# Optimization experiments

Measured on AMD Instinct MI355X. Metric: run time of the kernel, lower is better.

Reference implementation:

```python
import jax, jax.numpy as jnp
import numpy as np

K = 8  # kernel_size
COUT = 512


def setup_inputs() -> dict:
    key = jax.random.key(0)
    k1, k2, k3 = jax.random.split(key, 3)
    B, CIN, L = 8, 512, 2048
    x = jax.random.normal(k1, (B, CIN, L), dtype=jnp.float32)
    # nn.Linear(CIN, COUT*K) weight, scaled like kaiming-uniform-ish init
    W = jax.random.normal(k2, (COUT * K, CIN), dtype=jnp.float32) * (1.0 / np.sqrt(CIN))
    b = jax.random.normal(k3, (COUT,), dtype=jnp.float32)
    return {"x": x, "W": W, "b": b}


def reference(x, W, b):
    # x: (B, Cin, L); W: (Cout*K, Cin) with row layout j = k*Cout + co; b: (Cout,)
    B, Cin, L = x.shape
    # pointwise linear expand: (B, Cout*K, L)
    z = jnp.einsum('bcl,oc->bol', x, W)
    z = z.reshape(B, K, COUT, L)  # k-major channel layout
    # causal overlap-add fold: y[b,co,t] = sum_k z[b,k,co,t-k]
    y = z[:, 0]
    for k in range(1, K):  # small fixed kernel-size loop
        y = y.at[:, :, k:].add(z[:, k, :, : L - k])
    return y + b[None, :, None]
```

## Files before the change

### kernel.cpp

```cpp
#include <hip/hip_runtime.h>
#include <hip/hip_bf16.h>
#include <cstdint>
#include <cstddef>

#define CIN   512
#define COUT  512
#define LLEN  2048
#define BATCH 8
#define KTAP  8
#define LPAD  (LLEN + 8)

typedef __bf16 bf16x8_t __attribute__((ext_vector_type(8)));
typedef float  f32x4_t  __attribute__((ext_vector_type(4)));
typedef unsigned short u16x8_t __attribute__((ext_vector_type(8)));

__device__ __forceinline__ unsigned short f2bf(float f) {
  __bf16 h = (__bf16)f;
  return __builtin_bit_cast(unsigned short, h);
}

__device__ __forceinline__ void gl2lds16(unsigned short* lds, const unsigned short* g) {
  __builtin_amdgcn_global_load_lds(
      (const __attribute__((address_space(1))) unsigned int*)g,
      (__attribute__((address_space(3))) unsigned int*)lds,
      16, 0, 0);
}


__global__ void convert_w_kernel(const float4* __restrict__ W, u16x8_t* __restrict__ Wb) {
  int idx = blockIdx.x * 256 + threadIdx.x;
  float4 a = W[idx * 2], b = W[idx * 2 + 1];
  u16x8_t o;
  o[0] = f2bf(a.x); o[1] = f2bf(a.y); o[2] = f2bf(a.z); o[3] = f2bf(a.w);
  o[4] = f2bf(b.x); o[5] = f2bf(b.y); o[6] = f2bf(b.z); o[7] = f2bf(b.w);
  Wb[idx] = o;
}

__global__ __launch_bounds__(256) void transpose_x_kernel(
    const float* __restrict__ x, unsigned short* __restrict__ xtp) {
  __shared__ float tile[64][65];
  const int t  = threadIdx.x;
  const int b  = blockIdx.z;
  const int c0 = blockIdx.y * 64;
  const int l0 = blockIdx.x * 64;

  if (blockIdx.x == 0 && t < 64) {
    unsigned short* hp = xtp + ((size_t)b * LPAD + (t >> 3)) * CIN + c0 + (t & 7) * 8;
    *(u16x8_t*)hp = (u16x8_t){0, 0, 0, 0, 0, 0, 0, 0};
  }

  {
    const int cr = t >> 2;
    const int lv = (t & 3) * 16;
    const float* src = x + ((size_t)b * CIN + c0 + cr) * LLEN + l0 + lv;
#pragma unroll
    for (int i = 0; i < 4; ++i) {
      float4 v = *(const float4*)(src + 4 * i);
      tile[cr][lv + 4 * i + 0] = v.x;
      tile[cr][lv + 4 * i + 1] = v.y;
      tile[cr][lv + 4 * i + 2] = v.z;
      tile[cr][lv + 4 * i + 3] = v.w;
    }
  }
  __syncthreads();

  {
    const int l    = t >> 2;
    const int cseg = (t & 3) * 16;
    unsigned short ov[16];
#pragma unroll
    for (int u = 0; u < 16; ++u) ov[u] = f2bf(tile[cseg + u][l]);
    unsigned short* dst = xtp + ((size_t)b * LPAD + 8 + l0 + l) * CIN + c0 + cseg;
    *(u16x8_t*)dst       = *(const u16x8_t*)&ov[0];
    *(u16x8_t*)(dst + 8) = *(const u16x8_t*)&ov[8];
  }
}


__global__ __launch_bounds__(256) void conv_gemm_kernel(
    const unsigned short* __restrict__ Wb,
    const unsigned short* __restrict__ xtp,
    const float* __restrict__ bias,
    float* __restrict__ y)
{
  __shared__ __align__(16) unsigned short As[128 * 64];
  __shared__ __align__(16) unsigned short Bs[136 * 64];

  const int t    = threadIdx.x;
  const int lane = t & 63;
  const int wid  = t >> 6;
  const int wm   = wid & 1, wn = wid >> 1;
  const int l0   = blockIdx.x * 128;
  const int o0   = blockIdx.y * 128;
  const int b    = blockIdx.z;

  const int quad = lane >> 4;
  const int lrow = lane & 15;

  f32x4_t acc[4][4];
#pragma unroll
  for (int i = 0; i < 4; ++i)
#pragma unroll
    for (int j = 0; j < 4; ++j)
      acc[i][j] = (f32x4_t){0.f, 0.f, 0.f, 0.f};

  const int srow    = t >> 3;
  const int schunk  = (t & 7) ^ (srow & 7);
  const int lds_off = t * 8;

  const unsigned short* xb = xtp + (size_t)b * LPAD * CIN;

#pragma unroll 1
  for (int ct = 0; ct < 8; ++ct) {
    const int c0 = ct * 64;
    {
      const unsigned short* src = xb + (size_t)(l0 + srow) * CIN + c0 + schunk * 8;
#pragma unroll
      for (int rd = 0; rd < 4; ++rd)
        gl2lds16(Bs + lds_off + rd * 2048, src + (size_t)rd * 32 * CIN);
      if (t < 64) {
        const int r2 = 128 + (t >> 3);
        const int ch2 = (t & 7) ^ (r2 & 7);
        gl2lds16(Bs + 128 * 64 + t * 8,
                 xb + (size_t)(l0 + r2) * CIN + c0 + ch2 * 8);
      }
    }
#pragma unroll
    for (int k = 0; k < 8; ++k) {
      const unsigned short* asrc =
          Wb + (size_t)(k * COUT + o0 + srow) * CIN + c0 + schunk * 8;
#pragma unroll
      for (int rd = 0; rd < 4; ++rd)
        gl2lds16(As + lds_off + rd * 2048, asrc + (size_t)rd * 32 * CIN);
      __syncthreads();

#pragma unroll
      for (int h = 0; h < 2; ++h) {
        bf16x8_t af[4], bfr[4];
#pragma unroll
        for (int i = 0; i < 4; ++i) {
          int row  = wm * 64 + i * 16 + lrow;
          int slot = (h * 4 + quad) ^ (row & 7);
          af[i] = *(const bf16x8_t*)(As + row * 64 + slot * 8);
        }
#pragma unroll
        for (int j = 0; j < 4; ++j) {
          int row  = (8 - k) + wn * 64 + j * 16 + lrow;
          int slot = (h * 4 + quad) ^ (row & 7);
          bfr[j] = *(const bf16x8_t*)(Bs + row * 64 + slot * 8);
        }
#pragma unroll
        for (int i = 0; i < 4; ++i)
#pragma unroll
          for (int j = 0; j < 4; ++j)
            acc[i][j] = __builtin_amdgcn_mfma_f32_16x16x32_bf16(af[i], bfr[j], acc[i][j], 0, 0, 0);
      }
      __syncthreads();
    }
  }

#pragma unroll
  for (int i = 0; i < 4; ++i) {
    const int o_base = o0 + wm * 64 + i * 16 + quad * 4;
    const float4 bv = *(const float4*)(bias + o_base);
    const float bvr[4] = {bv.x, bv.y, bv.z, bv.w};
#pragma unroll
    for (int j = 0; j < 4; ++j) {
      const int l = l0 + wn * 64 + j * 16 + lrow;
#pragma unroll
      for (int r = 0; r < 4; ++r) {
        y[((size_t)b * COUT + o_base + r) * LLEN + l] = acc[i][j][r] + bvr[r];
      }
    }
  }
}


extern "C" void kernel_launch(void* const* d_in, const int* in_sizes, int n_in,
                              void* d_out, int out_size, void* d_ws, size_t ws_size,
                              hipStream_t stream) {
  const float* x    = (const float*)d_in[0];
  const float* W    = (const float*)d_in[1];
  const float* bias = (const float*)d_in[2];
  float* y          = (float*)d_out;

  unsigned short* xtp = (unsigned short*)d_ws;
  unsigned short* Wb  = (unsigned short*)((char*)d_ws +
                        (size_t)BATCH * LPAD * CIN * sizeof(unsigned short));

  convert_w_kernel<<<(KTAP * COUT * CIN / 8) / 256, 256, 0, stream>>>(
      (const float4*)W, (u16x8_t*)Wb);
  transpose_x_kernel<<<dim3(LLEN / 64, CIN / 64, BATCH), 256, 0, stream>>>(x, xtp);
  conv_gemm_kernel<<<dim3(LLEN / 128, COUT / 128, BATCH), 256, 0, stream>>>(
      Wb, xtp, bias, y);
}
```

Baseline: 150.0 us.

## Load weight fragments directly to registers with prefetch and merge prepass kernels

The GEMM kernel stops staging the weight tile through LDS. Each wave now loads its own A fragments from global memory straight into registers, one k-step ahead (double-buffered registers), which removes the per-tap LDS writes and two barriers per tap. The weight conversion and x transpose kernels are merged into one launch to save launch overhead. The cost is higher register pressure and uncoalesced 16-byte global reads of W that rely on L2/cache hits, with each wave reloading weights that the other wn wave also loads.

New measurement: 211.5 us. 1.41x slower.

```diff
diff --git a/kernel.cpp b/kernel.cpp
--- a/kernel.cpp
+++ b/kernel.cpp
@@ -26,25 +26,28 @@
       16, 0, 0);
 }
 
-
-__global__ void convert_w_kernel(const float4* __restrict__ W, u16x8_t* __restrict__ Wb) {
-  int idx = blockIdx.x * 256 + threadIdx.x;
-  float4 a = W[idx * 2], b = W[idx * 2 + 1];
-  u16x8_t o;
-  o[0] = f2bf(a.x); o[1] = f2bf(a.y); o[2] = f2bf(a.z); o[3] = f2bf(a.w);
-  o[4] = f2bf(b.x); o[5] = f2bf(b.y); o[6] = f2bf(b.z); o[7] = f2bf(b.w);
-  Wb[idx] = o;
-}
-
-__global__ __launch_bounds__(256) void transpose_x_kernel(
-    const float* __restrict__ x, unsigned short* __restrict__ xtp) {
+__global__ __launch_bounds__(256) void prepass_kernel(
+    const float* __restrict__ x, unsigned short* __restrict__ xtp,
+    const float4* __restrict__ W, u16x8_t* __restrict__ Wb) {
+  const int bid = blockIdx.x;
+  const int t   = threadIdx.x;
+
+  if (bid >= 2048) {
+    int idx = (bid - 2048) * 256 + t;
+    float4 a = W[idx * 2], b = W[idx * 2 + 1];
+    u16x8_t o;
+    o[0] = f2bf(a.x); o[1] = f2bf(a.y); o[2] = f2bf(a.z); o[3] = f2bf(a.w);
+    o[4] = f2bf(b.x); o[5] = f2bf(b.y); o[6] = f2bf(b.z); o[7] = f2bf(b.w);
+    Wb[idx] = o;
+    return;
+  }
+
   __shared__ float tile[64][65];
-  const int t  = threadIdx.x;
-  const int b  = blockIdx.z;
-  const int c0 = blockIdx.y * 64;
-  const int l0 = blockIdx.x * 64;
-
-  if (blockIdx.x == 0 && t < 64) {
+  const int b  = bid >> 8;
+  const int c0 = ((bid >> 5) & 7) * 64;
+  const int l0 = (bid & 31) * 64;
+
+  if ((bid & 31) == 0 && t < 64) {
     unsigned short* hp = xtp + ((size_t)b * LPAD + (t >> 3)) * CIN + c0 + (t & 7) * 8;
     *(u16x8_t*)hp = (u16x8_t){0, 0, 0, 0, 0, 0, 0, 0};
   }
@@ -63,7 +66,6 @@
     }
   }
   __syncthreads();
-
   {
     const int l    = t >> 2;
     const int cseg = (t & 3) * 16;
@@ -83,7 +85,6 @@
     const float* __restrict__ bias,
     float* __restrict__ y)
 {
-  __shared__ __align__(16) unsigned short As[128 * 64];
   __shared__ __align__(16) unsigned short Bs[136 * 64];
 
   const int t    = threadIdx.x;
@@ -110,39 +111,49 @@
 
   const unsigned short* xb = xtp + (size_t)b * LPAD * CIN;
 
+  const unsigned short* aW =
+      Wb + ((size_t)o0 + wm * 64 + lrow) * CIN + quad * 8;
+
+  bf16x8_t afc[2][4], afn[2][4];
+#pragma unroll
+  for (int h = 0; h < 2; ++h)
+#pragma unroll
+    for (int i = 0; i < 4; ++i)
+      afc[h][i] = *(const bf16x8_t*)(aW + h * 32 + i * 16 * CIN);
+
 #pragma unroll 1
   for (int ct = 0; ct < 8; ++ct) {
     const int c0 = ct * 64;
+    if (ct) __syncthreads();
     {
       const unsigned short* src = xb + (size_t)(l0 + srow) * CIN + c0 + schunk * 8;
 #pragma unroll
       for (int rd = 0; rd < 4; ++rd)
         gl2lds16(Bs + lds_off + rd * 2048, src + (size_t)rd * 32 * CIN);
       if (t < 64) {
-        const int r2 = 128 + (t >> 3);
+        const int r2  = 128 + (t >> 3);
         const int ch2 = (t & 7) ^ (r2 & 7);
         gl2lds16(Bs + 128 * 64 + t * 8,
                  xb + (size_t)(l0 + r2) * CIN + c0 + ch2 * 8);
       }
     }
+    __syncthreads();
+
 #pragma unroll
     for (int k = 0; k < 8; ++k) {
-      const unsigned short* asrc =
-          Wb + (size_t)(k * COUT + o0 + srow) * CIN + c0 + schunk * 8;
-#pragma unroll
-      for (int rd = 0; rd < 4; ++rd)
-        gl2lds16(As + lds_off + rd * 2048, asrc + (size_t)rd * 32 * CIN);
-      __syncthreads();
+      const int kk = ct * 8 + k;
+      const int kn = (kk + 1 < 64) ? kk + 1 : kk;
+      const unsigned short* an =
+          aW + (size_t)(kn & 7) * COUT * CIN + (kn >> 3) * 64;
+#pragma unroll
+      for (int h = 0; h < 2; ++h)
+#pragma unroll
+        for (int i = 0; i < 4; ++i)
+          afn[h][i] = *(const bf16x8_t*)(an + h * 32 + i * 16 * CIN);
 
 #pragma unroll
       for (int h = 0; h < 2; ++h) {
-        bf16x8_t af[4], bfr[4];
-#pragma unroll
-        for (int i = 0; i < 4; ++i) {
-          int row  = wm * 64 + i * 16 + lrow;
-          int slot = (h * 4 + quad) ^ (row & 7);
-          af[i] = *(const bf16x8_t*)(As + row * 64 + slot * 8);
-        }
+        bf16x8_t bfr[4];
 #pragma unroll
         for (int j = 0; j < 4; ++j) {
           int row  = (8 - k) + wn * 64 + j * 16 + lrow;
@@ -153,9 +164,13 @@
         for (int i = 0; i < 4; ++i)
 #pragma unroll
           for (int j = 0; j < 4; ++j)
-            acc[i][j] = __builtin_amdgcn_mfma_f32_16x16x32_bf16(af[i], bfr[j], acc[i][j], 0, 0, 0);
+            acc[i][j] = __builtin_amdgcn_mfma_f32_16x16x32_bf16(afc[h][i], bfr[j], acc[i][j], 0, 0, 0);
       }
-      __syncthreads();
+#pragma unroll
+      for (int h = 0; h < 2; ++h)
+#pragma unroll
+        for (int i = 0; i < 4; ++i)
+          afc[h][i] = afn[h][i];
     }
   }
 
@@ -188,9 +203,8 @@
   unsigned short* Wb  = (unsigned short*)((char*)d_ws +
                         (size_t)BATCH * LPAD * CIN * sizeof(unsigned short));
 
-  convert_w_kernel<<<(KTAP * COUT * CIN / 8) / 256, 256, 0, stream>>>(
-      (const float4*)W, (u16x8_t*)Wb);
-  transpose_x_kernel<<<dim3(LLEN / 64, CIN / 64, BATCH), 256, 0, stream>>>(x, xtp);
+  prepass_kernel<<<2048 + 1024, 256, 0, stream>>>(
+      x, xtp, (const float4*)W, (u16x8_t*)Wb);
   conv_gemm_kernel<<<dim3(LLEN / 128, COUT / 128, BATCH), 256, 0, stream>>>(
       Wb, xtp, bias, y);
 }
```
